# Optimization experiments

Hardware: AMD Instinct MI355X
Metric: run time of the kernel (lower is better)

The kernel has to match this reference:

```python
import jax, jax.numpy as jnp
import numpy as np

EPSILON = float(np.finfo(np.float32).tiny)
K = 64      # top-k edges to keep
TAU = 0.1   # gumbel-softmax temperature


def setup_inputs() -> dict:
    key = jax.random.key(0)
    k1, k2 = jax.random.split(key)
    B, N, E = 64, 256, 4
    scores = jax.random.normal(k1, (B, N, N, E), dtype=jnp.float32)
    # Gumbel(0,1) noise matching flat_scores shape [B*E, N*N]
    gumbel = jax.random.gumbel(k2, (B * E, N * N), dtype=jnp.float32)
    return {"scores": scores, "gumbel": gumbel}


def reference(scores, gumbel):
    B, N, _, E = scores.shape
    local_k = min(K, N * N)
    # [B, N, N, E] -> [B, E, N, N] -> [B*E, N*N]
    flat = scores.transpose(0, 3, 1, 2).reshape(B * E, N * N) + gumbel
    khot = jnp.zeros_like(flat)
    onehot = jnp.zeros_like(flat)

    def step(carry, _):
        flat, khot, onehot = carry
        khot_mask = jnp.maximum(1.0 - onehot, EPSILON)
        flat = flat + jnp.log(khot_mask)
        onehot = jax.nn.softmax(flat / TAU, axis=1)
        return (flat, khot + onehot, onehot), None

    (flat, khot, onehot), _ = jax.lax.scan(
        step, (flat, khot, onehot), None, length=local_k)

    # hard straight-through top-k
    _, ind = jax.lax.top_k(khot, local_k)                 # [B*E, local_k]
    rows = jnp.arange(khot.shape[0])[:, None]
    khot_hard = jnp.zeros_like(khot).at[rows, ind].set(1.0)
    res = khot_hard - jax.lax.stop_gradient(khot) + khot

    # [B*E, N*N] -> [B, E, N, N] -> [B, N, N, E]
    new_mask = res.reshape(B, E, N, N).transpose(0, 2, 3, 1)
    return new_mask
```

## Files before the change

kernel.cpp:

```cpp
#include <hip/hip_runtime.h>
#include <cfloat>
#include <math.h>

#define NROW   256
#define RLEN   65536
#define TPB    1024
#define VPT    64
#define REGS   8
#define MAXC   (TPB*REGS)
#define NITER  64
#define KSEL   64
#define THETA_OFF 8.0f
#define TCAP   256
#define LN_TGT 7.6246f
#define WGATE_D 1.4787e-8

__global__ void __launch_bounds__(TPB, 4)
GumbelSampler_2482491097709_kernel(const float* __restrict__ scores,
                                   const float* __restrict__ gumbel,
                                   float* __restrict__ out)
{
    __shared__ double s_Pd[2][16];
    __shared__ float s_EA[16];
    __shared__ float s_EB[16];
    __shared__ int   s_IC[16];
    __shared__ int   s_cnt;
    __shared__ int   s_selB;
    __shared__ int   s_selR;
    __shared__ int   s_tcnt;
    __shared__ int   s_tie[TCAP];
    __shared__ int   s_hist[4096];
    __shared__ int   cand_idx[MAXC];
    __shared__ float cand_kv[MAXC];

    const int tid  = threadIdx.x;
    const int lane = tid & 63;
    const int wid  = tid >> 6;

    const int q    = blockIdx.x;
    const int xcd  = q & 7;
    const int slot = q >> 3;
    const int b    = xcd * 8 + (slot & 7);
    const int e    = slot >> 3;
    const int r    = b * 4 + e;

    const float* __restrict__ sr = scores + (size_t)b * (RLEN * 4) + e;
    const float* __restrict__ gr = gumbel + (size_t)r * RLEN;

    float v[VPT];
    float lm = -FLT_MAX;
#pragma unroll
    for (int s = 0; s < VPT; ++s) {
        int p = tid + TPB * s;
        float x = sr[(size_t)p * 4] + gr[p];
        v[s] = x;
        lm = fmaxf(lm, x);
    }
#pragma unroll
    for (int s = 0; s < VPT; ++s) asm volatile("" : "+v"(v[s]));

#pragma unroll
    for (int o = 32; o; o >>= 1) lm = fmaxf(lm, __shfl_xor(lm, o));
    if (lane == 0) s_EA[wid] = lm;
    __syncthreads();
    float M0 = s_EA[lane & 15];
#pragma unroll
    for (int o = 8; o; o >>= 1) M0 = fmaxf(M0, __shfl_xor(M0, o));
    const float  C  = M0 * 10.0f;
    const double M0d = (double)M0;

    float theta = M0 - THETA_OFF;
    for (int probe = 0; probe < 12; ++probe) {
        int lc = 0;
#pragma unroll
        for (int s = 0; s < VPT; ++s) lc += (v[s] >= theta) ? 1 : 0;
#pragma unroll
        for (int o = 32; o; o >>= 1) lc += __shfl_xor(lc, o);
        if (lane == 0) s_IC[wid] = lc;
        __syncthreads();
        int cc = s_IC[lane & 15];
#pragma unroll
        for (int o = 8; o; o >>= 1) cc += __shfl_xor(cc, o);
        __syncthreads();
        if (cc > MAXC - 64)      theta += __logf((float)cc) - LN_TGT;
        else if (cc < KSEL)      theta -= LN_TGT - __logf((float)(cc < 1 ? 1 : cc));
        else break;
    }

    if (tid == 0) s_cnt = 0;
    __syncthreads();
    {
        float mu = -FLT_MAX, u = 0.f;
#pragma unroll
        for (int s = 0; s < VPT; ++s) {
            float val = v[s];
            bool pr = (val >= theta);
            unsigned long long m = __ballot(pr);
            if (pr) {
                int lead = __ffsll(m) - 1;
                int base = 0;
                if (lane == lead) base = atomicAdd(&s_cnt, (int)__popcll(m));
                base = __shfl(base, lead);
                int sl = base + (int)__popcll(m & ((1ull << lane) - 1ull));
                if (sl < MAXC) { cand_idx[sl] = tid + TPB * s; cand_kv[sl] = val; }
            } else {
                mu = fmaxf(mu, val);
                float yv = fmaf(val, 10.f, -C);
                if (yv > -87.f) u += __expf(yv);
            }
        }
#pragma unroll
        for (int o = 32; o; o >>= 1) {
            mu = fmaxf(mu, __shfl_xor(mu, o));
            u += __shfl_xor(u, o);
        }
        if (lane == 0) { s_EA[wid] = mu; s_EB[wid] = u; }
    }
    __syncthreads();
    int cnt = s_cnt;
    float Mu = s_EA[lane & 15], Uf = s_EB[lane & 15];
#pragma unroll
    for (int o = 8; o; o >>= 1) {
        Mu = fmaxf(Mu, __shfl_xor(Mu, o));
        Uf += __shfl_xor(Uf, o);
    }
    double Ud = (double)Uf;

    double w[REGS], kh[REGS];
#pragma unroll
    for (int j = 0; j < REGS; ++j) {
        int sl = tid + TPB * j;
        if (sl < cnt) w[j] = exp(10.0 * ((double)cand_kv[sl] - M0d));
        else          w[j] = 0.0;
        kh[j] = 0.0;
    }

    bool   noexp = false;
    double rcpS = 0.0, wT = 1e300;
    double Rsum = 0.0;
    double Ktrig = exp(fma(10.0, (double)Mu, -10.0 * M0d + 20.0));
    for (int t = 0; t < NITER; ++t) {
        const int pb = t & 1;
        double ls = 0.0;
#pragma unroll
        for (int j = 0; j < REGS; ++j) {
            int sl = tid + TPB * j;
            if (sl < cnt) {
                double wj = w[j];
                double o  = wj * rcpS;
                kh[j] += o;
                if (wj > wT) {
                    double m  = 1.0 - o;
                    double m2 = m * m;
                    double m4 = m2 * m2;
                    double m8 = m4 * m4;
                    wj *= m8 * m2;
                    w[j] = wj;
                }
                ls += wj;
            }
        }
#pragma unroll
        for (int o = 32; o; o >>= 1) ls += __shfl_xor(ls, o);
        if (lane == 0) s_Pd[pb][wid] = ls;
        __syncthreads();
        double S = s_Pd[pb][lane & 15];
#pragma unroll
        for (int o = 8; o; o >>= 1) S += __shfl_xor(S, o);
        S += Ud;
        rcpS = 1.0 / S;
        wT   = S * WGATE_D;

        if (!noexp && t < NITER - 1 && S < Ktrig) {
            double Lse  = fma(10.0, M0d, log(S));
            float thOld = theta;
            float thN   = (float)((Lse - 26.0) * 0.1);
            int   oldc  = cnt;
            float mu2 = -FLT_MAX, u2 = 0.f;
#pragma unroll 4
            for (int s = 0; s < VPT; ++s) {
                int p = tid + TPB * s;
                float val = sr[(size_t)p * 4] + gr[p];
                if (val < thOld) {
                    if (val >= thN) {
                        int sl = atomicAdd(&s_cnt, 1);
                        if (sl < MAXC) {
                            cand_idx[sl] = p;
                            cand_kv[sl]  = val;
                        }
                    } else {
                        mu2 = fmaxf(mu2, val);
                        float yv = fmaf(val, 10.f, -C);
                        if (yv > -87.f) u2 += __expf(yv);
                    }
                }
            }
#pragma unroll
            for (int o = 32; o; o >>= 1) {
                mu2 = fmaxf(mu2, __shfl_xor(mu2, o));
                u2 += __shfl_xor(u2, o);
            }
            if (lane == 0) { s_EA[wid] = mu2; s_EB[wid] = u2; }
            __syncthreads();
            int newc = s_cnt;
            if (newc > MAXC) {
                if (tid == 0) s_cnt = oldc;
                noexp = true;
            } else {
                float m2_ = s_EA[lane & 15], uu = s_EB[lane & 15];
#pragma unroll
                for (int o = 8; o; o >>= 1) {
                    m2_ = fmaxf(m2_, __shfl_xor(m2_, o));
                    uu += __shfl_xor(uu, o);
                }
                Mu = m2_; Ud = (double)uu; theta = thN;
                Ktrig = exp(fma(10.0, (double)Mu, -10.0 * M0d + 20.0));
#pragma unroll
                for (int j = 0; j < REGS; ++j) {
                    int sl = tid + TPB * j;
                    if (sl >= oldc && sl < newc) {
                        double wn = exp(10.0 * ((double)cand_kv[sl] - M0d));
                        w[j]  = wn;
                        kh[j] = wn * Rsum;
                    }
                }
                cnt = newc;
            }
        }
        Rsum += rcpS;
    }
#pragma unroll
    for (int j = 0; j < REGS; ++j) {
        int sl = tid + TPB * j;
        if (sl < cnt) {
            kh[j] += w[j] * rcpS;
            cand_kv[sl] = (float)kh[j];
        }
    }
    __syncthreads();

    unsigned prefix = 0;
    int Rrem = KSEL;
    for (int pass = 0; pass < 3; ++pass) {
        const int nbins = (pass == 2) ? 1024 : 2048;
        for (int i = tid; i < nbins; i += TPB) s_hist[i] = 0;
        __syncthreads();
#pragma unroll
        for (int j = 0; j < REGS; ++j) {
            int sl = tid + TPB * j;
            if (sl < cnt) {
                unsigned key = __float_as_uint(cand_kv[sl]);
                if (key != 0u) {
                    bool m; int bin;
                    if (pass == 0)      { m = true;                     bin = key >> 21; }
                    else if (pass == 1) { m = (key >> 21) == prefix;    bin = (key >> 10) & 2047; }
                    else                { m = (key >> 10) == prefix;    bin = key & 1023; }
                    if (m) atomicAdd(&s_hist[bin], 1);
                }
            }
        }
        __syncthreads();
        if (wid == 0) {
            int Rl = Rrem, found = -1;
            const int nch = nbins >> 6;
            const int c0 = (pass == 0) ? 23 : 0;
            for (int c = c0; c < nch && found < 0; ++c) {
                int bin = nbins - 1 - (c * 64 + lane);
                int h = s_hist[bin];
                int cum = h;
#pragma unroll
                for (int s2 = 1; s2 < 64; s2 <<= 1) {
                    int vv = __shfl_up(cum, s2);
                    if (lane >= s2) cum += vv;
                }
                unsigned long long mb = __ballot(cum >= Rl);
                if (mb) {
                    int fl = __ffsll(mb) - 1;
                    int cumex = __shfl(cum, fl) - __shfl(h, fl);
                    found = nbins - 1 - (c * 64 + fl);
                    Rl -= cumex;
                } else {
                    Rl -= __shfl(cum, 63);
                }
            }
            if (lane == 0) { s_selB = found; s_selR = Rl; }
        }
        __syncthreads();
        prefix = (prefix << ((pass == 2) ? 10 : 11)) | (unsigned)s_selB;
        Rrem = s_selR;
    }
    const unsigned Kstar = prefix;
    const int need = Rrem;

    if (tid == 0) s_tcnt = 0;
    __syncthreads();
#pragma unroll
    for (int j = 0; j < REGS; ++j) {
        int sl = tid + TPB * j;
        if (sl < cnt) {
            float khf = cand_kv[sl];
            unsigned key = __float_as_uint(khf);
            if (key > Kstar) {
                int p = cand_idx[sl];
                out[((size_t)b * RLEN + (size_t)p) * 4 + e] = (1.f - khf) + khf;
            } else if (key == Kstar) {
                int tp = atomicAdd(&s_tcnt, 1);
                if (tp < TCAP) s_tie[tp] = cand_idx[sl];
            }
        }
    }
    __syncthreads();
    if (wid == 0) {
        int T = s_tcnt < TCAP ? s_tcnt : TCAP;
        float kv = __uint_as_float(Kstar);
        float ov = (1.f - kv) + kv;
        for (int rdone = 0; rdone < need; ++rdone) {
            int bi = 0x7fffffff, bp = -1;
            for (int i = lane; i < T; i += 64) {
                int vv = s_tie[i];
                if (vv < bi) { bi = vv; bp = i; }
            }
#pragma unroll
            for (int s2 = 32; s2; s2 >>= 1) {
                int oi = __shfl_xor(bi, s2);
                int op = __shfl_xor(bp, s2);
                if (oi < bi) { bi = oi; bp = op; }
            }
            if (lane == 0 && bi != 0x7fffffff) {
                out[((size_t)b * RLEN + (size_t)bi) * 4 + e] = ov;
                s_tie[bp] = 0x7fffffff;
            }
        }
    }
}

extern "C" void kernel_launch(void* const* d_in, const int* in_sizes, int n_in,
                              void* d_out, int out_size, void* d_ws, size_t ws_size,
                              hipStream_t stream) {
    const float* scores = (const float*)d_in[0];
    const float* gumbel = (const float*)d_in[1];
    float* out = (float*)d_out;

    hipMemsetAsync(d_out, 0, (size_t)out_size * sizeof(float), stream);
    GumbelSampler_2482491097709_kernel<<<NROW, TPB, 0, stream>>>(scores, gumbel, out);
}
```

Before: 360.0 us.

## Use float reductions, float khot accumulators, and cheap exp in sampler loop

Replaces the double-precision block reduction of the softmax denominator with a float reduction. Before reducing, each partial sum is rescaled by a power of two derived from the previous total, and the code falls back to a double reduction only when the float sum underflows. The khot accumulators move from double to float, and the double exp calls become a range-reduced __expf plus ldexp. The aim is to cut FP64 shuffle and transcendental cost and register pressure in the 64-iteration loop. The risks are lost accumulation precision, which could change top-k tie ordering, and an extra branch-dependent sync path.

```diff
diff --git a/kernel.cpp b/kernel.cpp
--- a/kernel.cpp
+++ b/kernel.cpp
@@ -14,12 +14,22 @@
 #define TCAP   256
 #define LN_TGT 7.6246f
 #define WGATE_D 1.4787e-8
+#define SF_EPS  1e-18f
+
+
+__device__ __forceinline__ double wexp10(float val, double M0d) {
+    double y  = 10.0 * ((double)val - M0d);
+    double nf = floor(y * 1.4426950408889634);
+    float  fr = (float)(y - nf * 0.6931471805599453);
+    return ldexp((double)__expf(fr), (int)nf);
+}
 
 __global__ void __launch_bounds__(TPB, 4)
 GumbelSampler_2482491097709_kernel(const float* __restrict__ scores,
                                    const float* __restrict__ gumbel,
                                    float* __restrict__ out)
 {
+    __shared__ float  s_Pf[2][16];
     __shared__ double s_Pd[2][16];
     __shared__ float s_EA[16];
     __shared__ float s_EB[16];
@@ -66,7 +76,7 @@
     float M0 = s_EA[lane & 15];
 #pragma unroll
     for (int o = 8; o; o >>= 1) M0 = fmaxf(M0, __shfl_xor(M0, o));
-    const float  C  = M0 * 10.0f;
+    const float  C   = M0 * 10.0f;
     const double M0d = (double)M0;
 
     float theta = M0 - THETA_OFF;
@@ -126,19 +136,21 @@
     }
     double Ud = (double)Uf;
 
-    double w[REGS], kh[REGS];
+    double w[REGS];
+    float  kh[REGS];
 #pragma unroll
     for (int j = 0; j < REGS; ++j) {
         int sl = tid + TPB * j;
-        if (sl < cnt) w[j] = exp(10.0 * ((double)cand_kv[sl] - M0d));
+        if (sl < cnt) w[j] = wexp10(cand_kv[sl], M0d);
         else          w[j] = 0.0;
-        kh[j] = 0.0;
+        kh[j] = 0.f;
     }
 
     bool   noexp = false;
     double rcpS = 0.0, wT = 1e300;
     double Rsum = 0.0;
-    double Ktrig = exp(fma(10.0, (double)Mu, -10.0 * M0d + 20.0));
+    double Ktrig = wexp10(Mu + 2.0f, M0d);
+    int    kscale = 0;
     for (int t = 0; t < NITER; ++t) {
         const int pb = t & 1;
         double ls = 0.0;
@@ -148,7 +160,7 @@
             if (sl < cnt) {
                 double wj = w[j];
                 double o  = wj * rcpS;
-                kh[j] += o;
+                kh[j] += (float)o;
                 if (wj > wT) {
                     double m  = 1.0 - o;
                     double m2 = m * m;
@@ -160,16 +172,35 @@
                 ls += wj;
             }
         }
-#pragma unroll
-        for (int o = 32; o; o >>= 1) ls += __shfl_xor(ls, o);
-        if (lane == 0) s_Pd[pb][wid] = ls;
-        __syncthreads();
-        double S = s_Pd[pb][lane & 15];
-#pragma unroll
-        for (int o = 8; o; o >>= 1) S += __shfl_xor(S, o);
+        float lsf = (float)ldexp(ls, kscale);
+#pragma unroll
+        for (int o = 32; o; o >>= 1) lsf += __shfl_xor(lsf, o);
+        if (lane == 0) s_Pf[pb][wid] = lsf;
+        __syncthreads();
+        float Sf = s_Pf[pb][lane & 15];
+#pragma unroll
+        for (int o = 8; o; o >>= 1) Sf += __shfl_xor(Sf, o);
+        double S;
+        if (Sf >= SF_EPS) {
+            S = ldexp((double)Sf, -kscale);
+        } else {
+            double td = ls;
+#pragma unroll
+            for (int o = 32; o; o >>= 1) td += __shfl_xor(td, o);
+            if (lane == 0) s_Pd[pb][wid] = td;
+            __syncthreads();
+            double Sd = s_Pd[pb][lane & 15];
+#pragma unroll
+            for (int o = 8; o; o >>= 1) Sd += __shfl_xor(Sd, o);
+            S = Sd;
+        }
         S += Ud;
         rcpS = 1.0 / S;
         wT   = S * WGATE_D;
+        {
+            int ebits = (int)((__double_as_longlong(S) >> 52) & 0x7ff);
+            kscale = 1 - (ebits - 1023);
+        }
 
         if (!noexp && t < NITER - 1 && S < Ktrig) {
             double Lse  = fma(10.0, M0d, log(S));
@@ -214,14 +245,14 @@
                     uu += __shfl_xor(uu, o);
                 }
                 Mu = m2_; Ud = (double)uu; theta = thN;
-                Ktrig = exp(fma(10.0, (double)Mu, -10.0 * M0d + 20.0));
+                Ktrig = wexp10(Mu + 2.0f, M0d);
 #pragma unroll
                 for (int j = 0; j < REGS; ++j) {
                     int sl = tid + TPB * j;
                     if (sl >= oldc && sl < newc) {
-                        double wn = exp(10.0 * ((double)cand_kv[sl] - M0d));
+                        double wn = wexp10(cand_kv[sl], M0d);
                         w[j]  = wn;
-                        kh[j] = wn * Rsum;
+                        kh[j] = (float)(wn * Rsum);
                     }
                 }
                 cnt = newc;
@@ -233,8 +264,7 @@
     for (int j = 0; j < REGS; ++j) {
         int sl = tid + TPB * j;
         if (sl < cnt) {
-            kh[j] += w[j] * rcpS;
-            cand_kv[sl] = (float)kh[j];
+            cand_kv[sl] = kh[j] + (float)(w[j] * rcpS);
         }
     }
     __syncthreads();
```

After: 331.5 us. 1.09x faster.
